# Kernel optimization log

Measured on AMD Instinct MI355X. Metric: run time of the kernel, lower is better.

The kernel has to match this reference:

```python
import jax, jax.numpy as jnp
import numpy as np

N_FINE, N_COARSE, E_POOL, E_PP, C = 100000, 25000, 100000, 400000, 128

def setup_inputs() -> dict:
    key = jax.random.key(0)
    ks = jax.random.split(key, 24)
    d = {}
    d['x'] = jax.random.normal(ks[0], (N_FINE, C), jnp.float32)
    d['pool_src'] = jax.random.randint(ks[1], (E_POOL,), 0, N_FINE)
    d['pool_dst'] = jax.random.randint(ks[2], (E_POOL,), 0, N_COARSE)
    d['pool_attr'] = jax.random.uniform(ks[3], (E_POOL,), jnp.float32)
    d['pp_src'] = jax.random.randint(ks[4], (E_PP,), 0, N_COARSE)
    d['pp_dst'] = jax.random.randint(ks[5], (E_PP,), 0, N_COARSE)
    d['pp_attr'] = jax.random.uniform(ks[6], (E_PP,), jnp.float32)
    d['unpool_src'] = jax.random.randint(ks[7], (E_POOL,), 0, N_COARSE)
    d['unpool_dst'] = jax.random.randint(ks[8], (E_POOL,), 0, N_FINE)
    d['unpool_attr'] = jax.random.uniform(ks[9], (E_POOL,), jnp.float32)
    s = 1.0 / np.sqrt(C)
    for i in range(4):
        d[f'w{i+1}_self'] = jax.random.normal(ks[10 + 3 * i], (C, C), jnp.float32) * s
        d[f'w{i+1}_neigh'] = jax.random.normal(ks[11 + 3 * i], (C, C), jnp.float32) * s
        d[f'b{i+1}'] = jnp.zeros((C,), jnp.float32)
    d['n_coarse'] = N_COARSE
    d['n_fine'] = N_FINE
    return d

def reference(x, pool_src, pool_dst, pool_attr, pp_src, pp_dst, pp_attr,
              unpool_src, unpool_dst, unpool_attr,
              w1_self, w1_neigh, b1, w2_self, w2_neigh, b2,
              w3_self, w3_neigh, b3, w4_self, w4_neigh, b4,
              n_coarse, n_fine):
    # Pooling: edge-weighted scatter-add from fine nodes to coarse nodes.
    h = jax.ops.segment_sum(pool_attr[:, None] * x[pool_src], pool_dst,
                            num_segments=n_coarse)  # [n_coarse, C]
    def conv(h, ws, wn, b):
        # Message passing: gather src features, scale by edge_attr, scatter to dst.
        agg = jax.ops.segment_sum(pp_attr[:, None] * h[pp_src], pp_dst,
                                  num_segments=n_coarse)
        return jax.nn.relu(h @ ws + agg @ wn + b)
    h = conv(h, w1_self, w1_neigh, b1)
    h = conv(h, w2_self, w2_neigh, b2)
    h = conv(h, w3_self, w3_neigh, b3)
    h = conv(h, w4_self, w4_neigh, b4)
    # Unpooling: edge-weighted scatter-add from coarse back to fine nodes.
    out = jax.ops.segment_sum(unpool_attr[:, None] * h[unpool_src], unpool_dst,
                              num_segments=n_fine)  # [n_fine, C]
    return out
```

## Files before the change

### kernel.cpp

```cpp
#include <hip/hip_runtime.h>
#include <hip/hip_bf16.h>

#define C 128
#define NC 25000
#define SCHUNK 4096

typedef __attribute__((ext_vector_type(8))) short bf16x8;
typedef __attribute__((ext_vector_type(4))) float f32x4;

static __device__ __forceinline__ unsigned short f2bf(float x) {
    __hip_bfloat16 h = __float2bfloat16(x);
    return __builtin_bit_cast(unsigned short, h);
}
static __device__ __forceinline__ float bflo(unsigned int v) {
    return __builtin_bit_cast(float, v << 16);
}
static __device__ __forceinline__ float bfhi(unsigned int v) {
    return __builtin_bit_cast(float, v & 0xffff0000u);
}


__global__ __launch_bounds__(256) void hist_rank_k(
    const int* __restrict__ pl_dst, const int* __restrict__ pp_dst,
    const int* __restrict__ up_dst, int* __restrict__ cnt,
    int* __restrict__ rank, int Epl, int Epp, int Eup) {
    int i = blockIdx.x * blockDim.x + threadIdx.x;
    int cidx;
    if (i < Epl) {
        cidx = pl_dst[i];
    } else if (i < Epl + Epp) {
        cidx = NC + pp_dst[i - Epl];
    } else if (i < Epl + Epp + Eup) {
        cidx = 2 * NC + up_dst[i - Epl - Epp];
    } else return;
    rank[i] = atomicAdd(&cnt[cidx], 1);
}

__global__ __launch_bounds__(256) void fill2_k(
    const int* __restrict__ pl_src, const float* __restrict__ pl_attr,
    const int* __restrict__ pp_src, const float* __restrict__ pp_attr,
    const int* __restrict__ up_src, const float* __restrict__ up_attr,
    const int* __restrict__ pl_dst, const int* __restrict__ pp_dst,
    const int* __restrict__ up_dst,
    const int* __restrict__ off, const int* __restrict__ rank,
    int2* __restrict__ ep, int Epl, int Epp, int Eup) {
    int i = blockIdx.x * blockDim.x + threadIdx.x;
    int cidx, s; float a;
    if (i < Epl) {
        cidx = pl_dst[i]; s = pl_src[i]; a = pl_attr[i];
    } else if (i < Epl + Epp) {
        int j = i - Epl;
        cidx = NC + pp_dst[j]; s = pp_src[j]; a = pp_attr[j];
    } else if (i < Epl + Epp + Eup) {
        int j = i - Epl - Epp;
        cidx = 2 * NC + up_dst[j]; s = up_src[j]; a = up_attr[j];
    } else return;
    ep[off[cidx] + rank[i]] = make_int2(s, __float_as_int(a));
}


__global__ __launch_bounds__(256) void reduce_k(const int* __restrict__ cnt,
                                                int* __restrict__ bsum, int n) {
    __shared__ int wpart[4];
    int base = blockIdx.x * SCHUNK;
    int tid = threadIdx.x;
    int end = base + SCHUNK; if (end > n) end = n;
    int s = 0;
    for (int i = base + tid; i < end; i += 256) s += cnt[i];
#pragma unroll
    for (int d = 32; d > 0; d >>= 1) s += __shfl_down(s, d, 64);
    if ((tid & 63) == 0) wpart[tid >> 6] = s;
    __syncthreads();
    if (tid == 0) bsum[blockIdx.x] = wpart[0] + wpart[1] + wpart[2] + wpart[3];
}

__global__ void scan_bsum_k(int* __restrict__ bsum, int* __restrict__ off,
                            int nb, int n) {
    int lane = threadIdx.x;
    int orig = (lane < nb) ? bsum[lane] : 0;
    int incl = orig;
#pragma unroll
    for (int d = 1; d < 64; d <<= 1) {
        int t = __shfl_up(incl, d, 64);
        if (lane >= d) incl += t;
    }
    if (lane < nb) bsum[lane] = incl - orig;
    if (lane == 63) off[n] = incl;
}

__global__ __launch_bounds__(1024) void scan_blk_k(const int* __restrict__ cnt,
                                                   const int* __restrict__ bexcl,
                                                   int* __restrict__ off, int n) {
    __shared__ int wsum[16];
    const int tid = threadIdx.x, lane = tid & 63, wid = tid >> 6;
    int idx0 = blockIdx.x * SCHUNK + tid * 4;
    int v[4]; int s = 0;
#pragma unroll
    for (int j = 0; j < 4; ++j) { v[j] = (idx0 + j < n) ? cnt[idx0 + j] : 0; s += v[j]; }
    int sc = s;
#pragma unroll
    for (int d = 1; d < 64; d <<= 1) {
        int t = __shfl_up(sc, d, 64);
        if (lane >= d) sc += t;
    }
    if (lane == 63) wsum[wid] = sc;
    __syncthreads();
    if (wid == 0) {
        int ws = (lane < 16) ? wsum[lane] : 0;
#pragma unroll
        for (int d = 1; d < 16; d <<= 1) {
            int t = __shfl_up(ws, d, 64);
            if (lane >= d) ws += t;
        }
        if (lane < 16) wsum[lane] = ws;
    }
    __syncthreads();
    int wave_off = (wid > 0) ? wsum[wid - 1] : 0;
    int excl = bexcl[blockIdx.x] + wave_off + sc - s;
#pragma unroll
    for (int j = 0; j < 4; ++j) {
        if (idx0 + j < n) off[idx0 + j] = excl;
        excl += v[j];
    }
}

template<bool IN_BF16, bool OUT_BF16>
__global__ __launch_bounds__(256) void gather_k(
    const void* __restrict__ in_, const int* __restrict__ off,
    const int2* __restrict__ ep, void* __restrict__ out_, int n) {
    int node = (blockIdx.x * 256 + threadIdx.x) >> 4;
    if (node >= n) return;
    int lane = threadIdx.x & 15;
    int e0 = off[node], e1 = off[node + 1];
    float acc[8];
#pragma unroll
    for (int j = 0; j < 8; ++j) acc[j] = 0.f;

    const unsigned int* inb = (const unsigned int*)in_;
    const float* inf = (const float*)in_;

    int e = e0;
    for (; e + 1 < e1; e += 2) {
        int2 p0 = ep[e], p1 = ep[e + 1];
        float a0 = __int_as_float(p0.y), a1 = __int_as_float(p1.y);
        if (IN_BF16) {
            uint4 v0 = *(const uint4*)(inb + (size_t)p0.x * 64 + lane * 4);
            uint4 v1 = *(const uint4*)(inb + (size_t)p1.x * 64 + lane * 4);
            acc[0] = fmaf(a0, bflo(v0.x), acc[0]); acc[1] = fmaf(a0, bfhi(v0.x), acc[1]);
            acc[2] = fmaf(a0, bflo(v0.y), acc[2]); acc[3] = fmaf(a0, bfhi(v0.y), acc[3]);
            acc[4] = fmaf(a0, bflo(v0.z), acc[4]); acc[5] = fmaf(a0, bfhi(v0.z), acc[5]);
            acc[6] = fmaf(a0, bflo(v0.w), acc[6]); acc[7] = fmaf(a0, bfhi(v0.w), acc[7]);
            acc[0] = fmaf(a1, bflo(v1.x), acc[0]); acc[1] = fmaf(a1, bfhi(v1.x), acc[1]);
            acc[2] = fmaf(a1, bflo(v1.y), acc[2]); acc[3] = fmaf(a1, bfhi(v1.y), acc[3]);
            acc[4] = fmaf(a1, bflo(v1.z), acc[4]); acc[5] = fmaf(a1, bfhi(v1.z), acc[5]);
            acc[6] = fmaf(a1, bflo(v1.w), acc[6]); acc[7] = fmaf(a1, bfhi(v1.w), acc[7]);
        } else {
            const float* r0 = inf + (size_t)p0.x * C + lane * 8;
            const float* r1 = inf + (size_t)p1.x * C + lane * 8;
            float4 u0 = *(const float4*)r0, u1 = *(const float4*)(r0 + 4);
            float4 w0 = *(const float4*)r1, w1 = *(const float4*)(r1 + 4);
            acc[0] = fmaf(a0, u0.x, acc[0]); acc[1] = fmaf(a0, u0.y, acc[1]);
            acc[2] = fmaf(a0, u0.z, acc[2]); acc[3] = fmaf(a0, u0.w, acc[3]);
            acc[4] = fmaf(a0, u1.x, acc[4]); acc[5] = fmaf(a0, u1.y, acc[5]);
            acc[6] = fmaf(a0, u1.z, acc[6]); acc[7] = fmaf(a0, u1.w, acc[7]);
            acc[0] = fmaf(a1, w0.x, acc[0]); acc[1] = fmaf(a1, w0.y, acc[1]);
            acc[2] = fmaf(a1, w0.z, acc[2]); acc[3] = fmaf(a1, w0.w, acc[3]);
            acc[4] = fmaf(a1, w1.x, acc[4]); acc[5] = fmaf(a1, w1.y, acc[5]);
            acc[6] = fmaf(a1, w1.z, acc[6]); acc[7] = fmaf(a1, w1.w, acc[7]);
        }
    }
    if (e < e1) {
        int2 p0 = ep[e];
        float a0 = __int_as_float(p0.y);
        if (IN_BF16) {
            uint4 v0 = *(const uint4*)(inb + (size_t)p0.x * 64 + lane * 4);
            acc[0] = fmaf(a0, bflo(v0.x), acc[0]); acc[1] = fmaf(a0, bfhi(v0.x), acc[1]);
            acc[2] = fmaf(a0, bflo(v0.y), acc[2]); acc[3] = fmaf(a0, bfhi(v0.y), acc[3]);
            acc[4] = fmaf(a0, bflo(v0.z), acc[4]); acc[5] = fmaf(a0, bfhi(v0.z), acc[5]);
            acc[6] = fmaf(a0, bflo(v0.w), acc[6]); acc[7] = fmaf(a0, bfhi(v0.w), acc[7]);
        } else {
            const float* r0 = inf + (size_t)p0.x * C + lane * 8;
            float4 u0 = *(const float4*)r0, u1 = *(const float4*)(r0 + 4);
            acc[0] = fmaf(a0, u0.x, acc[0]); acc[1] = fmaf(a0, u0.y, acc[1]);
            acc[2] = fmaf(a0, u0.z, acc[2]); acc[3] = fmaf(a0, u0.w, acc[3]);
            acc[4] = fmaf(a0, u1.x, acc[4]); acc[5] = fmaf(a0, u1.y, acc[5]);
            acc[6] = fmaf(a0, u1.z, acc[6]); acc[7] = fmaf(a0, u1.w, acc[7]);
        }
    }

    if (OUT_BF16) {
        uint4 r;
        r.x = (unsigned)f2bf(acc[0]) | ((unsigned)f2bf(acc[1]) << 16);
        r.y = (unsigned)f2bf(acc[2]) | ((unsigned)f2bf(acc[3]) << 16);
        r.z = (unsigned)f2bf(acc[4]) | ((unsigned)f2bf(acc[5]) << 16);
        r.w = (unsigned)f2bf(acc[6]) | ((unsigned)f2bf(acc[7]) << 16);
        *(uint4*)((unsigned int*)out_ + (size_t)node * 64 + lane * 4) = r;
    } else {
        float* ob = (float*)out_ + (size_t)node * C + lane * 8;
        *(float4*)ob = make_float4(acc[0], acc[1], acc[2], acc[3]);
        *(float4*)(ob + 4) = make_float4(acc[4], acc[5], acc[6], acc[7]);
    }
}

__global__ __launch_bounds__(256) void wprep4_k(
    const float* __restrict__ w0s, const float* __restrict__ w0n,
    const float* __restrict__ w1s, const float* __restrict__ w1n,
    const float* __restrict__ w2s, const float* __restrict__ w2n,
    const float* __restrict__ w3s, const float* __restrict__ w3n,
    unsigned short* __restrict__ wt) {
    int i = blockIdx.x * blockDim.x + threadIdx.x;
    if (i >= 4 * 128 * 256) return;
    int l = i >> 15;
    int r = i & 32767;
    int col = r >> 8, k = r & 255;
    const float* ws = (l == 0) ? w0s : (l == 1) ? w1s : (l == 2) ? w2s : w3s;
    const float* wn = (l == 0) ? w0n : (l == 1) ? w1n : (l == 2) ? w2n : w3n;
    float v = (k < 128) ? ws[k * 128 + col] : wn[(k - 128) * 128 + col];
    wt[i] = f2bf(v);
}

__global__ __launch_bounds__(256, 2) void conv_mfma_k(
    const unsigned short* __restrict__ hin, const unsigned short* __restrict__ agg,
    const unsigned short* __restrict__ wt, const float* __restrict__ bias,
    unsigned short* __restrict__ hout, int n) {
    const int wv = threadIdx.x >> 6;
    const int lane = threadIdx.x & 63;
    const int col0 = wv * 32;
    const int r0 = blockIdx.x * 64;
    if (r0 >= n) return;
    const int q = lane >> 4;
    const int lr = lane & 15;

    bf16x8 bfr[2][8];
#pragma unroll
    for (int nt = 0; nt < 2; ++nt) {
        int col = col0 + nt * 16 + lr;
#pragma unroll
        for (int kk = 0; kk < 8; ++kk)
            bfr[nt][kk] = *(const bf16x8*)(wt + col * 256 + kk * 32 + q * 8);
    }

    f32x4 acc[4][2];
#pragma unroll
    for (int m = 0; m < 4; ++m)
#pragma unroll
        for (int nt = 0; nt < 2; ++nt) acc[m][nt] = (f32x4)(0.f);

    int rowb[4];
#pragma unroll
    for (int m = 0; m < 4; ++m) {
        int row = r0 + m * 16 + lr;
        rowb[m] = (row < n) ? row : (n - 1);
    }

#pragma unroll
    for (int kk = 0; kk < 8; ++kk) {
        const unsigned short* srcbase = (kk < 4) ? hin : agg;
        const int koff = (kk & 3) * 32 + q * 8;
#pragma unroll
        for (int m = 0; m < 4; ++m) {
            bf16x8 a = *(const bf16x8*)(srcbase + (size_t)rowb[m] * C + koff);
#pragma unroll
            for (int nt = 0; nt < 2; ++nt)
                acc[m][nt] = __builtin_amdgcn_mfma_f32_16x16x32_bf16(
                    a, bfr[nt][kk], acc[m][nt], 0, 0, 0);
        }
    }

#pragma unroll
    for (int nt = 0; nt < 2; ++nt) {
        int col = col0 + nt * 16 + lr;
        float bv = bias[col];
#pragma unroll
        for (int m = 0; m < 4; ++m) {
#pragma unroll
            for (int r = 0; r < 4; ++r) {
                int row = r0 + m * 16 + q * 4 + r;
                if (row < n) {
                    float v = acc[m][nt][r] + bv;
                    hout[(size_t)row * C + col] = f2bf(v > 0.f ? v : 0.f);
                }
            }
        }
    }
}


extern "C" void kernel_launch(void* const* d_in, const int* in_sizes, int n_in,
                              void* d_out, int out_size, void* d_ws, size_t ws_size,
                              hipStream_t stream) {
    const float* x         = (const float*)d_in[0];
    const int*   pool_src  = (const int*)d_in[1];
    const int*   pool_dst  = (const int*)d_in[2];
    const float* pool_attr = (const float*)d_in[3];
    const int*   pp_src    = (const int*)d_in[4];
    const int*   pp_dst    = (const int*)d_in[5];
    const float* pp_attr   = (const float*)d_in[6];
    const int*   up_src    = (const int*)d_in[7];
    const int*   up_dst    = (const int*)d_in[8];
    const float* up_attr   = (const float*)d_in[9];
    const float* w[12];
    for (int i = 0; i < 12; ++i) w[i] = (const float*)d_in[10 + i];

    const int E_pool = in_sizes[1];
    const int E_pp   = in_sizes[4];
    const int E_up   = in_sizes[7];
    const int NF     = in_sizes[0] / C;
    const int TOT    = 2 * NC + NF;
    const int TE     = E_pool + E_pp + E_up;

    unsigned short* h   = (unsigned short*)d_ws;
    unsigned short* h2  = h + (size_t)NC * C;
    unsigned short* agg = h2 + (size_t)NC * C;
    int*  cnt_all = (int*)(agg + (size_t)NC * C);
    int*  off_all = cnt_all + TOT;
    int*  rank    = off_all + TOT + 1;
    int2* ep_all  = (int2*)(rank + TE);
    unsigned short* wt = (unsigned short*)(ep_all + TE);
    int* bsum = (int*)(wt + 4 * 128 * 256);

    const int* pl_off = off_all;
    const int* pp_off = off_all + NC;
    const int* up_off = off_all + 2 * NC;

    const int TB = 256;

    wprep4_k<<<(4 * 128 * 256 + TB - 1) / TB, TB, 0, stream>>>(
        w[0], w[1], w[3], w[4], w[6], w[7], w[9], w[10], wt);

    hipMemsetAsync(cnt_all, 0, (size_t)TOT * sizeof(int), stream);
    hist_rank_k<<<(TE + TB - 1) / TB, TB, 0, stream>>>(
        pool_dst, pp_dst, up_dst, cnt_all, rank, E_pool, E_pp, E_up);
    {
        int nb = (TOT + SCHUNK - 1) / SCHUNK;
        reduce_k<<<nb, 256, 0, stream>>>(cnt_all, bsum, TOT);
        scan_bsum_k<<<1, 64, 0, stream>>>(bsum, off_all, nb, TOT);
        scan_blk_k<<<nb, 1024, 0, stream>>>(cnt_all, bsum, off_all, TOT);
    }
    fill2_k<<<(TE + TB - 1) / TB, TB, 0, stream>>>(
        pool_src, pool_attr, pp_src, pp_attr, up_src, up_attr,
        pool_dst, pp_dst, up_dst, off_all, rank, ep_all, E_pool, E_pp, E_up);

    gather_k<false, true><<<((size_t)NC * 16 + 255) / 256, 256, 0, stream>>>(
        x, pl_off, ep_all, h, NC);

    unsigned short* hcur = h;
    unsigned short* halt = h2;
    const int mtiles = (NC + 63) / 64;
    for (int l = 0; l < 4; ++l) {
        gather_k<true, true><<<((size_t)NC * 16 + 255) / 256, 256, 0, stream>>>(
            hcur, pp_off, ep_all, agg, NC);
        conv_mfma_k<<<mtiles, 256, 0, stream>>>(
            hcur, agg, wt + (size_t)l * 128 * 256, w[3 * l + 2], halt, NC);
        unsigned short* t = hcur; hcur = halt; halt = t;
    }

    gather_k<true, false><<<((size_t)NF * 16 + 255) / 256, 256, 0, stream>>>(
        hcur, up_off, ep_all, (float*)d_out, NF);
}
```

Baseline: 217.9 us.

## Fuse neighbor gather into MFMA conv kernel via LDS aggregate tile

Each conv layer now computes the edge-weighted neighbor aggregation for its 64-row tile directly into a swizzled shared-memory buffer, then runs the MFMA matmul reading agg from LDS. This removes a separate gather launch per layer and the global write and read of the agg tensor. The weight prep and count zeroing are merged into one kernel, and hist_rank packs the destination index into rank so fill no longer rereads the dst arrays. In exchange, the per-block gather uses only 16 lanes per row and adds LDS pressure, which may lower gather parallelism and occupancy.

```diff
diff --git a/kernel.cpp b/kernel.cpp
--- a/kernel.cpp
+++ b/kernel.cpp
@@ -17,6 +17,28 @@
 }
 static __device__ __forceinline__ float bfhi(unsigned int v) {
     return __builtin_bit_cast(float, v & 0xffff0000u);
+}
+
+__global__ __launch_bounds__(256) void prep_k(
+    const float* __restrict__ w0s, const float* __restrict__ w0n,
+    const float* __restrict__ w1s, const float* __restrict__ w1n,
+    const float* __restrict__ w2s, const float* __restrict__ w2n,
+    const float* __restrict__ w3s, const float* __restrict__ w3n,
+    unsigned short* __restrict__ wt, int* __restrict__ cnt, int tot) {
+    int b = blockIdx.x;
+    if (b < 512) {
+        int i = b * 256 + threadIdx.x;
+        int l = i >> 15;
+        int r = i & 32767;
+        int col = r >> 8, k = r & 255;
+        const float* ws = (l == 0) ? w0s : (l == 1) ? w1s : (l == 2) ? w2s : w3s;
+        const float* wn = (l == 0) ? w0n : (l == 1) ? w1n : (l == 2) ? w2n : w3n;
+        float v = (k < 128) ? ws[k * 128 + col] : wn[(k - 128) * 128 + col];
+        wt[i] = f2bf(v);
+    } else {
+        int i = (b - 512) * 256 + threadIdx.x;
+        if (i < tot) cnt[i] = 0;
+    }
 }
 
 
@@ -33,29 +55,31 @@
     } else if (i < Epl + Epp + Eup) {
         cidx = 2 * NC + up_dst[i - Epl - Epp];
     } else return;
-    rank[i] = atomicAdd(&cnt[cidx], 1);
+    int p = atomicAdd(&cnt[cidx], 1);
+    rank[i] = (p << 18) | cidx;
 }
 
 __global__ __launch_bounds__(256) void fill2_k(
     const int* __restrict__ pl_src, const float* __restrict__ pl_attr,
     const int* __restrict__ pp_src, const float* __restrict__ pp_attr,
     const int* __restrict__ up_src, const float* __restrict__ up_attr,
-    const int* __restrict__ pl_dst, const int* __restrict__ pp_dst,
-    const int* __restrict__ up_dst,
     const int* __restrict__ off, const int* __restrict__ rank,
     int2* __restrict__ ep, int Epl, int Epp, int Eup) {
     int i = blockIdx.x * blockDim.x + threadIdx.x;
-    int cidx, s; float a;
+    int s; float a;
     if (i < Epl) {
-        cidx = pl_dst[i]; s = pl_src[i]; a = pl_attr[i];
+        s = pl_src[i]; a = pl_attr[i];
     } else if (i < Epl + Epp) {
         int j = i - Epl;
-        cidx = NC + pp_dst[j]; s = pp_src[j]; a = pp_attr[j];
+        s = pp_src[j]; a = pp_attr[j];
     } else if (i < Epl + Epp + Eup) {
         int j = i - Epl - Epp;
-        cidx = 2 * NC + up_dst[j]; s = up_src[j]; a = up_attr[j];
+        s = up_src[j]; a = up_attr[j];
     } else return;
-    ep[off[cidx] + rank[i]] = make_int2(s, __float_as_int(a));
+    unsigned v = (unsigned)rank[i];
+    int cidx = v & 0x3FFFF;
+    int p = (int)(v >> 18);
+    ep[off[cidx] + p] = make_int2(s, __float_as_int(a));
 }
 
 
@@ -202,32 +226,17 @@
     }
 }
 
-__global__ __launch_bounds__(256) void wprep4_k(
-    const float* __restrict__ w0s, const float* __restrict__ w0n,
-    const float* __restrict__ w1s, const float* __restrict__ w1n,
-    const float* __restrict__ w2s, const float* __restrict__ w2n,
-    const float* __restrict__ w3s, const float* __restrict__ w3n,
-    unsigned short* __restrict__ wt) {
-    int i = blockIdx.x * blockDim.x + threadIdx.x;
-    if (i >= 4 * 128 * 256) return;
-    int l = i >> 15;
-    int r = i & 32767;
-    int col = r >> 8, k = r & 255;
-    const float* ws = (l == 0) ? w0s : (l == 1) ? w1s : (l == 2) ? w2s : w3s;
-    const float* wn = (l == 0) ? w0n : (l == 1) ? w1n : (l == 2) ? w2n : w3n;
-    float v = (k < 128) ? ws[k * 128 + col] : wn[(k - 128) * 128 + col];
-    wt[i] = f2bf(v);
-}
-
-__global__ __launch_bounds__(256, 2) void conv_mfma_k(
-    const unsigned short* __restrict__ hin, const unsigned short* __restrict__ agg,
+__global__ __launch_bounds__(256, 2) void gconv_k(
+    const unsigned short* __restrict__ hin,
+    const int* __restrict__ off, const int2* __restrict__ ep,
     const unsigned short* __restrict__ wt, const float* __restrict__ bias,
     unsigned short* __restrict__ hout, int n) {
-    const int wv = threadIdx.x >> 6;
-    const int lane = threadIdx.x & 63;
+    __shared__ unsigned int aggs[64 * 64];
+    const int tid = threadIdx.x;
+    const int r0 = blockIdx.x * 64;
+    const int wv = tid >> 6;
+    const int lane = tid & 63;
     const int col0 = wv * 32;
-    const int r0 = blockIdx.x * 64;
-    if (r0 >= n) return;
     const int q = lane >> 4;
     const int lr = lane & 15;
 
@@ -240,11 +249,57 @@
             bfr[nt][kk] = *(const bf16x8*)(wt + col * 256 + kk * 32 + q * 8);
     }
 
-    f32x4 acc[4][2];
+    {
+        const int qw = tid >> 4, l16 = tid & 15;
+        const unsigned int* inb = (const unsigned int*)hin;
+        for (int rr = qw; rr < 64; rr += 16) {
+            int node = r0 + rr;
+            float acc[8];
+#pragma unroll
+            for (int j = 0; j < 8; ++j) acc[j] = 0.f;
+            if (node < n) {
+                int e0 = off[node], e1 = off[node + 1];
+                int e = e0;
+                for (; e + 1 < e1; e += 2) {
+                    int2 p0 = ep[e], p1 = ep[e + 1];
+                    float a0 = __int_as_float(p0.y), a1 = __int_as_float(p1.y);
+                    uint4 v0 = *(const uint4*)(inb + (size_t)p0.x * 64 + l16 * 4);
+                    uint4 v1 = *(const uint4*)(inb + (size_t)p1.x * 64 + l16 * 4);
+                    acc[0] = fmaf(a0, bflo(v0.x), acc[0]); acc[1] = fmaf(a0, bfhi(v0.x), acc[1]);
+                    acc[2] = fmaf(a0, bflo(v0.y), acc[2]); acc[3] = fmaf(a0, bfhi(v0.y), acc[3]);
+                    acc[4] = fmaf(a0, bflo(v0.z), acc[4]); acc[5] = fmaf(a0, bfhi(v0.z), acc[5]);
+                    acc[6] = fmaf(a0, bflo(v0.w), acc[6]); acc[7] = fmaf(a0, bfhi(v0.w), acc[7]);
+                    acc[0] = fmaf(a1, bflo(v1.x), acc[0]); acc[1] = fmaf(a1, bfhi(v1.x), acc[1]);
+                    acc[2] = fmaf(a1, bflo(v1.y), acc[2]); acc[3] = fmaf(a1, bfhi(v1.y), acc[3]);
+                    acc[4] = fmaf(a1, bflo(v1.z), acc[4]); acc[5] = fmaf(a1, bfhi(v1.z), acc[5]);
+                    acc[6] = fmaf(a1, bflo(v1.w), acc[6]); acc[7] = fmaf(a1, bfhi(v1.w), acc[7]);
+                }
+                if (e < e1) {
+                    int2 p0 = ep[e];
+                    float a0 = __int_as_float(p0.y);
+                    uint4 v0 = *(const uint4*)(inb + (size_t)p0.x * 64 + l16 * 4);
+                    acc[0] = fmaf(a0, bflo(v0.x), acc[0]); acc[1] = fmaf(a0, bfhi(v0.x), acc[1]);
+                    acc[2] = fmaf(a0, bflo(v0.y), acc[2]); acc[3] = fmaf(a0, bfhi(v0.y), acc[3]);
+                    acc[4] = fmaf(a0, bflo(v0.z), acc[4]); acc[5] = fmaf(a0, bfhi(v0.z), acc[5]);
+                    acc[6] = fmaf(a0, bflo(v0.w), acc[6]); acc[7] = fmaf(a0, bfhi(v0.w), acc[7]);
+                }
+            }
+            uint4 r;
+            r.x = (unsigned)f2bf(acc[0]) | ((unsigned)f2bf(acc[1]) << 16);
+            r.y = (unsigned)f2bf(acc[2]) | ((unsigned)f2bf(acc[3]) << 16);
+            r.z = (unsigned)f2bf(acc[4]) | ((unsigned)f2bf(acc[5]) << 16);
+            r.w = (unsigned)f2bf(acc[6]) | ((unsigned)f2bf(acc[7]) << 16);
+            *(uint4*)(aggs + rr * 64 + ((l16 ^ (rr & 15)) << 2)) = r;
+        }
+    }
+    __syncthreads();
+
+    if (r0 >= n) return;
+    f32x4 acc2[4][2];
 #pragma unroll
     for (int m = 0; m < 4; ++m)
 #pragma unroll
-        for (int nt = 0; nt < 2; ++nt) acc[m][nt] = (f32x4)(0.f);
+        for (int nt = 0; nt < 2; ++nt) acc2[m][nt] = (f32x4)(0.f);
 
     int rowb[4];
 #pragma unroll
@@ -255,15 +310,20 @@
 
 #pragma unroll
     for (int kk = 0; kk < 8; ++kk) {
-        const unsigned short* srcbase = (kk < 4) ? hin : agg;
-        const int koff = (kk & 3) * 32 + q * 8;
 #pragma unroll
         for (int m = 0; m < 4; ++m) {
-            bf16x8 a = *(const bf16x8*)(srcbase + (size_t)rowb[m] * C + koff);
+            bf16x8 a;
+            if (kk < 4) {
+                a = *(const bf16x8*)(hin + (size_t)rowb[m] * C + kk * 32 + q * 8);
+            } else {
+                int row_local = m * 16 + lr;
+                int g = ((kk - 4) * 4 + q) ^ (row_local & 15);
+                a = *(const bf16x8*)(aggs + row_local * 64 + g * 4);
+            }
 #pragma unroll
             for (int nt = 0; nt < 2; ++nt)
-                acc[m][nt] = __builtin_amdgcn_mfma_f32_16x16x32_bf16(
-                    a, bfr[nt][kk], acc[m][nt], 0, 0, 0);
+                acc2[m][nt] = __builtin_amdgcn_mfma_f32_16x16x32_bf16(
+                    a, bfr[nt][kk], acc2[m][nt], 0, 0, 0);
         }
     }
 
@@ -277,7 +337,7 @@
             for (int r = 0; r < 4; ++r) {
                 int row = r0 + m * 16 + q * 4 + r;
                 if (row < n) {
-                    float v = acc[m][nt][r] + bv;
+                    float v = acc2[m][nt][r] + bv;
                     hout[(size_t)row * C + col] = f2bf(v > 0.f ? v : 0.f);
                 }
             }
@@ -311,8 +371,7 @@
 
     unsigned short* h   = (unsigned short*)d_ws;
     unsigned short* h2  = h + (size_t)NC * C;
-    unsigned short* agg = h2 + (size_t)NC * C;
-    int*  cnt_all = (int*)(agg + (size_t)NC * C);
+    int*  cnt_all = (int*)(h2 + (size_t)NC * C);
     int*  off_all = cnt_all + TOT;
     int*  rank    = off_all + TOT + 1;
     int2* ep_all  = (int2*)(rank + TE);
@@ -325,10 +384,9 @@
 
     const int TB = 256;
 
-    wprep4_k<<<(4 * 128 * 256 + TB - 1) / TB, TB, 0, stream>>>(
-        w[0], w[1], w[3], w[4], w[6], w[7], w[9], w[10], wt);
-
-    hipMemsetAsync(cnt_all, 0, (size_t)TOT * sizeof(int), stream);
+    prep_k<<<512 + (TOT + TB - 1) / TB, TB, 0, stream>>>(
+        w[0], w[1], w[3], w[4], w[6], w[7], w[9], w[10], wt, cnt_all, TOT);
+
     hist_rank_k<<<(TE + TB - 1) / TB, TB, 0, stream>>>(
         pool_dst, pp_dst, up_dst, cnt_all, rank, E_pool, E_pp, E_up);
     {
@@ -339,7 +397,7 @@
     }
     fill2_k<<<(TE + TB - 1) / TB, TB, 0, stream>>>(
         pool_src, pool_attr, pp_src, pp_attr, up_src, up_attr,
-        pool_dst, pp_dst, up_dst, off_all, rank, ep_all, E_pool, E_pp, E_up);
+        off_all, rank, ep_all, E_pool, E_pp, E_up);
 
     gather_k<false, true><<<((size_t)NC * 16 + 255) / 256, 256, 0, stream>>>(
         x, pl_off, ep_all, h, NC);
@@ -348,10 +406,8 @@
     unsigned short* halt = h2;
     const int mtiles = (NC + 63) / 64;
     for (int l = 0; l < 4; ++l) {
-        gather_k<true, true><<<((size_t)NC * 16 + 255) / 256, 256, 0, stream>>>(
-            hcur, pp_off, ep_all, agg, NC);
-        conv_mfma_k<<<mtiles, 256, 0, stream>>>(
-            hcur, agg, wt + (size_t)l * 128 * 256, w[3 * l + 2], halt, NC);
+        gconv_k<<<mtiles, 256, 0, stream>>>(
+            hcur, pp_off, ep_all, wt + (size_t)l * 128 * 256, w[3 * l + 2], halt, NC);
         unsigned short* t = hcur; hcur = halt; halt = t;
     }
 
```

Result: slower. 272.0 us (+24.8%).
